# Kernel optimization log

Measured on AMD Instinct MI355X. Metric: run time of the kernel, lower is better.

Reference implementation:

```python
import jax, jax.numpy as jnp
import numpy as np

N_NODES = 50000
N_EDGES = 800000
D_FEAT = 128
D_EMB = 128


def setup_inputs() -> dict:
    key = jax.random.key(0)
    k1, k2, k3, k4, k5 = jax.random.split(key, 5)
    feature = jax.random.normal(k1, (N_NODES, D_FEAT), dtype=jnp.float32)
    edge_src = jax.random.randint(k2, (N_EDGES,), 0, N_NODES, dtype=jnp.int32)
    edge_dst = jax.random.randint(k3, (N_EDGES,), 0, N_NODES, dtype=jnp.int32)
    edge_w = jax.random.uniform(k4, (N_EDGES,), dtype=jnp.float32)
    # reset_parameters: uniform(-stdv, stdv), stdv = 1/sqrt(embedding_size)
    stdv = 1.0 / np.sqrt(D_EMB)
    weight = jax.random.uniform(k5, (D_FEAT, D_EMB), dtype=jnp.float32,
                                minval=-stdv, maxval=stdv)
    return {"feature": feature, "edge_src": edge_src, "edge_dst": edge_dst,
            "edge_w": edge_w, "weight": weight}


def reference(feature, edge_src, edge_dst, edge_w, weight):
    # spmm(adj, feature): out[dst] += w * feature[src]
    msgs = edge_w[:, None] * feature[edge_src]          # [E, D_FEAT]
    agg = jax.ops.segment_sum(msgs, edge_dst, num_segments=feature.shape[0])
    # residual blend then dense projection
    blended = 0.5 * agg + 0.5 * feature                  # [N, D_FEAT]
    return blended @ weight                              # [N, D_EMB]
```

## Files before the change

kernel.cpp:

```cpp
#include <hip/hip_runtime.h>

#define N_NODES 50000
#define N_EDGES 800000
#define D 128
#define NBUCK 196
#define CAP 4800
#define CHUNK 4096
#define PA_BLKS ((N_EDGES + CHUNK - 1) / CHUNK)
#define FB_BLKS 12500
#define WT_BLKS 64

typedef __attribute__((ext_vector_type(8))) short short8;
typedef __attribute__((ext_vector_type(4))) float f32x4;

__device__ __forceinline__ unsigned short f2bf(float f) {
    unsigned u = __float_as_uint(f);
    u += 0x7fff + ((u >> 16) & 1);
    return (unsigned short)(u >> 16);
}
__device__ __forceinline__ float lo16f(unsigned u) { return __uint_as_float(u << 16); }
__device__ __forceinline__ float hi16f(unsigned u) { return __uint_as_float(u & 0xffff0000u); }

__global__ __launch_bounds__(256) void prep_passA(
    const float2* __restrict__ feat2, unsigned* __restrict__ fb,
    const float* __restrict__ W, unsigned short* __restrict__ Wt,
    const int* __restrict__ esrc, const int* __restrict__ edst,
    const float* __restrict__ ew, int* __restrict__ gcur,
    uint2* __restrict__ tmp) {
    __shared__ int lh[NBUCK], lbase[NBUCK], lcur[NBUCK];
    int blk = blockIdx.x, t = threadIdx.x;

    if (blk >= PA_BLKS) {
        int b2 = blk - PA_BLKS;
        if (b2 < FB_BLKS) {
            int i = b2 * 256 + t;
            float2 f = feat2[i];
            fb[i] = (unsigned)f2bf(f.x) | ((unsigned)f2bf(f.y) << 16);
        } else {
            int idx = (b2 - FB_BLKS) * 256 + t;
            int n = idx >> 7, k = idx & 127;
            Wt[idx] = f2bf(W[k * 128 + n]);
        }
        return;
    }

    for (int i = t; i < NBUCK; i += 256) lh[i] = 0;
    __syncthreads();
    int e0 = blk * CHUNK;
    unsigned key[16];
    float wv[16];
#pragma unroll
    for (int j = 0; j < 16; ++j) {
        int e = e0 + j * 256 + t;
        if (e < N_EDGES) {
            int src = esrc[e], dd = edst[e];
            key[j] = (unsigned)src | ((unsigned)(dd & 255) << 16) |
                     ((unsigned)(dd >> 8) << 24);
            wv[j] = ew[e];
            atomicAdd(&lh[dd >> 8], 1);
        } else key[j] = 0xff000000u;
    }
    __syncthreads();
    for (int i = t; i < NBUCK; i += 256) {
        lbase[i] = atomicAdd(&gcur[i], lh[i]);
        lcur[i] = 0;
    }
    __syncthreads();
#pragma unroll
    for (int j = 0; j < 16; ++j) {
        int b = key[j] >> 24;
        if (b < NBUCK) {
            int r = atomicAdd(&lcur[b], 1);
            tmp[(size_t)b * CAP + lbase[b] + r] =
                make_uint2(key[j] & 0x00ffffffu, __float_as_uint(wv[j]));
        }
    }
}

__global__ __launch_bounds__(256) void passB(const int* __restrict__ gcur,
                                             const uint2* __restrict__ tmp,
                                             int* __restrict__ offsets,
                                             uint2* __restrict__ sw) {
    __shared__ int hist[256], ps[256];
    __shared__ int sbase, scnt;
    int b = blockIdx.x, t = threadIdx.x;

    int gv = (t < NBUCK) ? gcur[t] : 0;
    ps[t] = gv;
    __syncthreads();
    for (int off = 1; off < 256; off <<= 1) {
        int x = (t >= off) ? ps[t - off] : 0;
        __syncthreads();
        ps[t] += x;
        __syncthreads();
    }
    if (t == b) { sbase = ps[t] - gv; scnt = gv; }
    hist[t] = 0;
    __syncthreads();
    int base = sbase, cnt = scnt;
    const uint2* seg = tmp + (size_t)b * CAP;

    for (int i = t; i < cnt; i += 256) atomicAdd(&hist[seg[i].x >> 16], 1);
    __syncthreads();
    int h = hist[t];
    ps[t] = h;
    __syncthreads();
    for (int off = 1; off < 256; off <<= 1) {
        int x = (t >= off) ? ps[t - off] : 0;
        __syncthreads();
        ps[t] += x;
        __syncthreads();
    }
    int o = base + ps[t] - h;
    int node = b * 256 + t;
    if (node < N_NODES) offsets[node] = o;
    if (b == NBUCK - 1 && t == 0) offsets[N_NODES] = N_EDGES;
    __syncthreads();
    hist[t] = o;
    __syncthreads();
    for (int i = t; i < cnt; i += 256) {
        uint2 u = seg[i];
        int pos = atomicAdd(&hist[u.x >> 16], 1);
        sw[pos] = make_uint2(u.x & 0xffffu, u.y);
    }
}

__global__ __launch_bounds__(256, 2) void agg_gemm(const int* __restrict__ offsets,
                                                   const uint2* __restrict__ sw,
                                                   const unsigned* __restrict__ fb,
                                                   const unsigned short* __restrict__ Wt,
                                                   float* __restrict__ out) {
    __shared__ unsigned Arows[16][68];
    int wave = threadIdx.x >> 6;
    int lane = threadIdx.x & 63;
    int lsh = lane << 2;
    int row0 = blockIdx.x * 16;

#pragma unroll 1
    for (int i = 0; i < 4; ++i) {
        int n = __builtin_amdgcn_readfirstlane(row0 + wave * 4 + i);
        int b = offsets[n], e2 = offsets[n + 1];
        unsigned us = fb[(size_t)n * 64 + lane];
        float ax = 0.f, ay = 0.f;
        int nb = (e2 - b + 15) >> 4;

#pragma unroll 1
        for (int t = 0; t < nb; ++t) {
            int base = b + t * 16;
            int rem = e2 - base;
            uint2 p[16];
            unsigned voff[16];
#pragma unroll
            for (int j = 0; j < 16; ++j) {
                int idx = (j < rem) ? j : rem - 1;
                p[j] = sw[base + idx];
                voff[j] = (p[j].x << 8) | (unsigned)lsh;
            }
            unsigned u[16];
#pragma unroll
            for (int j = 0; j < 16; ++j)
                asm volatile("global_load_dword %0, %1, %2"
                             : "=v"(u[j]) : "v"(voff[j]), "s"(fb));
            asm volatile("s_waitcnt vmcnt(0)"
                         : "+v"(u[0]), "+v"(u[1]), "+v"(u[2]), "+v"(u[3]),
                           "+v"(u[4]), "+v"(u[5]), "+v"(u[6]), "+v"(u[7]),
                           "+v"(u[8]), "+v"(u[9]), "+v"(u[10]), "+v"(u[11]),
                           "+v"(u[12]), "+v"(u[13]), "+v"(u[14]), "+v"(u[15])
                         :: "memory");
#pragma unroll
            for (int j = 0; j < 16; ++j) {
                float w = (j < rem) ? __uint_as_float(p[j].y) : 0.f;
                ax += w * lo16f(u[j]);
                ay += w * hi16f(u[j]);
            }
        }
        float rx = 0.5f * (ax + lo16f(us));
        float ry = 0.5f * (ay + hi16f(us));
        Arows[wave * 4 + i][lane] = (unsigned)f2bf(rx) | ((unsigned)f2bf(ry) << 16);
    }
    __syncthreads();

    int quad = lane >> 4;
    int col  = lane & 15;
    short8 a[4];
#pragma unroll
    for (int kk = 0; kk < 4; ++kk)
        a[kk] = *reinterpret_cast<const short8*>(&Arows[col][kk * 16 + quad * 4]);

#pragma unroll
    for (int ii = 0; ii < 2; ++ii) {
        int n0 = wave * 2 + ii;
        const short8* bp = reinterpret_cast<const short8*>(Wt) + ((n0 * 16 + col) * 16 + quad);
        f32x4 acc = {0.f, 0.f, 0.f, 0.f};
        acc = __builtin_amdgcn_mfma_f32_16x16x32_bf16(a[0], bp[0],  acc, 0, 0, 0);
        acc = __builtin_amdgcn_mfma_f32_16x16x32_bf16(a[1], bp[4],  acc, 0, 0, 0);
        acc = __builtin_amdgcn_mfma_f32_16x16x32_bf16(a[2], bp[8],  acc, 0, 0, 0);
        acc = __builtin_amdgcn_mfma_f32_16x16x32_bf16(a[3], bp[12], acc, 0, 0, 0);
#pragma unroll
        for (int rr = 0; rr < 4; ++rr)
            out[(size_t)(row0 + quad * 4 + rr) * D + n0 * 16 + col] = acc[rr];
    }
}

extern "C" void kernel_launch(void* const* d_in, const int* in_sizes, int n_in,
                              void* d_out, int out_size, void* d_ws, size_t ws_size,
                              hipStream_t stream) {
    const float* feat = (const float*)d_in[0];
    const int*   esrc = (const int*)d_in[1];
    const int*   edst = (const int*)d_in[2];
    const float* ew   = (const float*)d_in[3];
    const float* W    = (const float*)d_in[4];
    float*       out  = (float*)d_out;

    char* ws = (char*)d_ws;
    uint2*          sw      = (uint2*)(ws + 0);
    unsigned*       fb      = (unsigned*)(ws + 6400000);
    int*            offsets = (int*)(ws + 19200000);
    unsigned short* Wt      = (unsigned short*)(ws + 19400064);
    int*            gcur    = (int*)(ws + 19432832);
    uint2* tmp = (uint2*)d_out;

    hipMemsetAsync(gcur, 0, NBUCK * sizeof(int), stream);
    prep_passA<<<PA_BLKS + FB_BLKS + WT_BLKS, 256, 0, stream>>>(
        (const float2*)feat, fb, W, Wt, esrc, edst, ew, gcur, tmp);
    passB<<<NBUCK, 256, 0, stream>>>(gcur, tmp, offsets, sw);
    agg_gemm<<<N_NODES / 16, 256, 0, stream>>>(offsets, sw, fb, Wt, out);
}
```

Baseline: 152.2 us.

## Assign one wave per node, load edge lists once and broadcast via readlane

The aggregation+GEMM kernel now launches 1024-thread blocks so each of 16 waves handles one node instead of each wave looping over four nodes. Each wave loads up to 32 edge records in one coalesced load and broadcasts them with readlane, replacing 16 redundant per-lane loads of the same record. The gather batch grows from 16 to 32 in-flight loads per wave to raise memory-level parallelism. The costs are higher register pressure, 12 waves sitting idle during the MFMA stage, and larger blocks that may lower occupancy flexibility.

New measurement: 162.2 us. 6.5% more time.

```diff
diff --git a/kernel.cpp b/kernel.cpp
--- a/kernel.cpp
+++ b/kernel.cpp
@@ -125,80 +125,81 @@
     }
 }
 
-__global__ __launch_bounds__(256, 2) void agg_gemm(const int* __restrict__ offsets,
-                                                   const uint2* __restrict__ sw,
-                                                   const unsigned* __restrict__ fb,
-                                                   const unsigned short* __restrict__ Wt,
-                                                   float* __restrict__ out) {
+__global__ __launch_bounds__(1024, 2) void agg_gemm(const int* __restrict__ offsets,
+                                                    const uint2* __restrict__ sw,
+                                                    const unsigned* __restrict__ fb,
+                                                    const unsigned short* __restrict__ Wt,
+                                                    float* __restrict__ out) {
     __shared__ unsigned Arows[16][68];
     int wave = threadIdx.x >> 6;
     int lane = threadIdx.x & 63;
-    int lsh = lane << 2;
+    unsigned lsh = (unsigned)(lane << 2);
     int row0 = blockIdx.x * 16;
 
-#pragma unroll 1
-    for (int i = 0; i < 4; ++i) {
-        int n = __builtin_amdgcn_readfirstlane(row0 + wave * 4 + i);
+    {
+        int n = __builtin_amdgcn_readfirstlane(row0 + wave);
         int b = offsets[n], e2 = offsets[n + 1];
         unsigned us = fb[(size_t)n * 64 + lane];
         float ax = 0.f, ay = 0.f;
-        int nb = (e2 - b + 15) >> 4;
-
+        int e = b;
 #pragma unroll 1
-        for (int t = 0; t < nb; ++t) {
-            int base = b + t * 16;
-            int rem = e2 - base;
-            uint2 p[16];
-            unsigned voff[16];
-#pragma unroll
-            for (int j = 0; j < 16; ++j) {
-                int idx = (j < rem) ? j : rem - 1;
-                p[j] = sw[base + idx];
-                voff[j] = (p[j].x << 8) | (unsigned)lsh;
+        while (e < e2) {
+            int rem = e2 - e;
+            int li = lane & 31;
+            uint2 sv = sw[e + (li < rem ? li : rem - 1)];
+            unsigned u[32];
+#pragma unroll
+            for (int j = 0; j < 32; ++j) {
+                unsigned voff = (__builtin_amdgcn_readlane(sv.x, j) << 8) | lsh;
+                asm volatile("global_load_dword %0, %1, %2"
+                             : "=v"(u[j]) : "v"(voff), "s"(fb));
             }
-            unsigned u[16];
-#pragma unroll
-            for (int j = 0; j < 16; ++j)
-                asm volatile("global_load_dword %0, %1, %2"
-                             : "=v"(u[j]) : "v"(voff[j]), "s"(fb));
             asm volatile("s_waitcnt vmcnt(0)"
                          : "+v"(u[0]), "+v"(u[1]), "+v"(u[2]), "+v"(u[3]),
                            "+v"(u[4]), "+v"(u[5]), "+v"(u[6]), "+v"(u[7]),
                            "+v"(u[8]), "+v"(u[9]), "+v"(u[10]), "+v"(u[11]),
-                           "+v"(u[12]), "+v"(u[13]), "+v"(u[14]), "+v"(u[15])
+                           "+v"(u[12]), "+v"(u[13]), "+v"(u[14]), "+v"(u[15]),
+                           "+v"(u[16]), "+v"(u[17]), "+v"(u[18]), "+v"(u[19]),
+                           "+v"(u[20]), "+v"(u[21]), "+v"(u[22]), "+v"(u[23]),
+                           "+v"(u[24]), "+v"(u[25]), "+v"(u[26]), "+v"(u[27]),
+                           "+v"(u[28]), "+v"(u[29]), "+v"(u[30]), "+v"(u[31])
                          :: "memory");
 #pragma unroll
-            for (int j = 0; j < 16; ++j) {
-                float w = (j < rem) ? __uint_as_float(p[j].y) : 0.f;
+            for (int j = 0; j < 32; ++j) {
+                float w = (j < rem)
+                    ? __uint_as_float(__builtin_amdgcn_readlane(sv.y, j)) : 0.f;
                 ax += w * lo16f(u[j]);
                 ay += w * hi16f(u[j]);
             }
+            e += 32;
         }
         float rx = 0.5f * (ax + lo16f(us));
         float ry = 0.5f * (ay + hi16f(us));
-        Arows[wave * 4 + i][lane] = (unsigned)f2bf(rx) | ((unsigned)f2bf(ry) << 16);
-    }
-    __syncthreads();
-
-    int quad = lane >> 4;
-    int col  = lane & 15;
-    short8 a[4];
-#pragma unroll
-    for (int kk = 0; kk < 4; ++kk)
-        a[kk] = *reinterpret_cast<const short8*>(&Arows[col][kk * 16 + quad * 4]);
-
-#pragma unroll
-    for (int ii = 0; ii < 2; ++ii) {
-        int n0 = wave * 2 + ii;
-        const short8* bp = reinterpret_cast<const short8*>(Wt) + ((n0 * 16 + col) * 16 + quad);
-        f32x4 acc = {0.f, 0.f, 0.f, 0.f};
-        acc = __builtin_amdgcn_mfma_f32_16x16x32_bf16(a[0], bp[0],  acc, 0, 0, 0);
-        acc = __builtin_amdgcn_mfma_f32_16x16x32_bf16(a[1], bp[4],  acc, 0, 0, 0);
-        acc = __builtin_amdgcn_mfma_f32_16x16x32_bf16(a[2], bp[8],  acc, 0, 0, 0);
-        acc = __builtin_amdgcn_mfma_f32_16x16x32_bf16(a[3], bp[12], acc, 0, 0, 0);
-#pragma unroll
-        for (int rr = 0; rr < 4; ++rr)
-            out[(size_t)(row0 + quad * 4 + rr) * D + n0 * 16 + col] = acc[rr];
+        Arows[wave][lane] = (unsigned)f2bf(rx) | ((unsigned)f2bf(ry) << 16);
+    }
+    __syncthreads();
+
+    if (wave < 4) {
+        int quad = lane >> 4;
+        int col  = lane & 15;
+        short8 a[4];
+#pragma unroll
+        for (int kk = 0; kk < 4; ++kk)
+            a[kk] = *reinterpret_cast<const short8*>(&Arows[col][kk * 16 + quad * 4]);
+
+#pragma unroll
+        for (int ii = 0; ii < 2; ++ii) {
+            int n0 = wave * 2 + ii;
+            const short8* bp = reinterpret_cast<const short8*>(Wt) + ((n0 * 16 + col) * 16 + quad);
+            f32x4 acc = {0.f, 0.f, 0.f, 0.f};
+            acc = __builtin_amdgcn_mfma_f32_16x16x32_bf16(a[0], bp[0],  acc, 0, 0, 0);
+            acc = __builtin_amdgcn_mfma_f32_16x16x32_bf16(a[1], bp[4],  acc, 0, 0, 0);
+            acc = __builtin_amdgcn_mfma_f32_16x16x32_bf16(a[2], bp[8],  acc, 0, 0, 0);
+            acc = __builtin_amdgcn_mfma_f32_16x16x32_bf16(a[3], bp[12], acc, 0, 0, 0);
+#pragma unroll
+            for (int rr = 0; rr < 4; ++rr)
+                out[(size_t)(row0 + quad * 4 + rr) * D + n0 * 16 + col] = acc[rr];
+        }
     }
 }
 
@@ -224,5 +225,5 @@
     prep_passA<<<PA_BLKS + FB_BLKS + WT_BLKS, 256, 0, stream>>>(
         (const float2*)feat, fb, W, Wt, esrc, edst, ew, gcur, tmp);
     passB<<<NBUCK, 256, 0, stream>>>(gcur, tmp, offsets, sw);
-    agg_gemm<<<N_NODES / 16, 256, 0, stream>>>(offsets, sw, fb, Wt, out);
-}
+    agg_gemm<<<N_NODES / 16, 1024, 0, stream>>>(offsets, sw, fb, Wt, out);
+}
```
